# Kernel optimization log

Measured on AMD Instinct MI355X. Metric: run time of the kernel, lower is better.

Reference implementation:

```python
import jax, jax.numpy as jnp
import numpy as np

N = 50000      # nodes per graph batch (per siamese side)
E = 500000     # edges per side
F_IN = 128     # input_channels
H = 128        # hidden_channels
OUT = 2        # output_channels
G = 512        # number of graphs in the batch


def setup_inputs() -> dict:
    key = jax.random.key(0)
    ks = jax.random.split(key, 16)

    def lin_w(k, fan_in, shape):
        lim = 1.0 / np.sqrt(fan_in)
        return jax.random.uniform(k, shape, jnp.float32, -lim, lim)

    return {
        "x1": jax.random.normal(ks[0], (N, F_IN), jnp.float32),
        "x2": jax.random.normal(ks[1], (N, F_IN), jnp.float32),
        "edge_index1": jax.random.randint(ks[2], (2, E), 0, N, jnp.int32),
        "edge_index2": jax.random.randint(ks[3], (2, E), 0, N, jnp.int32),
        "batch1": jnp.sort(jax.random.randint(ks[4], (N,), 0, G, jnp.int32)),
        "batch2": jnp.sort(jax.random.randint(ks[5], (N,), 0, G, jnp.int32)),
        "W1": lin_w(ks[6], F_IN, (F_IN, H)), "b1": jnp.zeros((H,), jnp.float32),
        "W2": lin_w(ks[7], H, (H, H)),       "b2": jnp.zeros((H,), jnp.float32),
        "W3": lin_w(ks[8], H, (H, H)),       "b3": jnp.zeros((H,), jnp.float32),
        "Wc1": lin_w(ks[9], 2 * H, (2 * H, 4 * H)), "bc1": jnp.zeros((4 * H,), jnp.float32),
        "Wc2": lin_w(ks[10], 4 * H, (4 * H, 2 * H)), "bc2": jnp.zeros((2 * H,), jnp.float32),
        "Wc3": lin_w(ks[11], 2 * H, (2 * H, OUT)),   "bc3": jnp.zeros((OUT,), jnp.float32),
        "num_graphs": G,
    }


def _gcn_layer(x, W, b, src, dst, dinv):
    # PyG GCNConv: linear transform, then deg^{-1/2} A_hat deg^{-1/2} aggregation + bias
    h = x @ W
    msg = h[src] * (dinv[src] * dinv[dst])[:, None]   # [E+N, H]
    return jax.ops.segment_sum(msg, dst, num_segments=x.shape[0]) + b


def _forward_once(x, edge_index, batch, W1, b1, W2, b2, W3, b3, num_graphs):
    n = x.shape[0]
    loop = jnp.arange(n, dtype=edge_index.dtype)
    src = jnp.concatenate([edge_index[0], loop])      # add self-loops
    dst = jnp.concatenate([edge_index[1], loop])
    deg = jax.ops.segment_sum(jnp.ones_like(dst, dtype=x.dtype), dst, num_segments=n)
    dinv = jax.lax.rsqrt(deg)                          # deg >= 1 due to self-loops
    h = jax.nn.relu(_gcn_layer(x, W1, b1, src, dst, dinv))
    h = jax.nn.relu(_gcn_layer(h, W2, b2, src, dst, dinv))
    h = _gcn_layer(h, W3, b3, src, dst, dinv)
    # global_mean_pool over batch indices
    s = jax.ops.segment_sum(h, batch, num_segments=num_graphs)
    cnt = jax.ops.segment_sum(jnp.ones((n,), x.dtype), batch, num_segments=num_graphs)
    return s / jnp.maximum(cnt, 1.0)[:, None]


def reference(x1, x2, edge_index1, edge_index2, batch1, batch2,
              W1, b1, W2, b2, W3, b3, Wc1, bc1, Wc2, bc2, Wc3, bc3, num_graphs):
    g1 = _forward_once(x1, edge_index1, batch1, W1, b1, W2, b2, W3, b3, num_graphs)
    g2 = _forward_once(x2, edge_index2, batch2, W1, b1, W2, b2, W3, b3, num_graphs)
    z = jnp.concatenate([g1, g2], axis=1)             # [G, 2H]
    z = jax.nn.relu(z @ Wc1 + bc1)
    z = jax.nn.relu(z @ Wc2 + bc2)
    # dropout p=0.5 is identity at eval time
    return z @ Wc3 + bc3                               # [G, OUT]
```

## Files before the change

### kernel.cpp

```cpp
#include <hip/hip_runtime.h>
#include <math.h>

#define N_NODES 50000
#define E_EDGES 500000
#define HDIM    128
#define OUTC    2
#define NGRAPH  512

typedef _Float16 f16x8 __attribute__((ext_vector_type(8)));
typedef float    f32x4 __attribute__((ext_vector_type(4)));

__global__ void k_prep(const float* __restrict__ W1, const float* __restrict__ W2,
                       _Float16* __restrict__ w1hi, _Float16* __restrict__ w1lo,
                       _Float16* __restrict__ w2hi, _Float16* __restrict__ w2lo) {
    int i = blockIdx.x * blockDim.x + threadIdx.x;
    int stride = gridDim.x * blockDim.x;
    for (int j = i; j < 128 * 128; j += stride) {
        int n = j >> 7, k = j & 127;
        float v = W1[k * 128 + n];
        _Float16 h = (_Float16)v;
        w1hi[j] = h; w1lo[j] = (_Float16)(v - (float)h);
        v = W2[k * 128 + n];
        h = (_Float16)v;
        w2hi[j] = h; w2lo[j] = (_Float16)(v - (float)h);
    }
}

__global__ void k_hist(const int* __restrict__ d0, const int* __restrict__ d1,
                       int ecnt, int off1, int* __restrict__ cnt) {
    int i = blockIdx.x * blockDim.x + threadIdx.x;
    int stride = gridDim.x * blockDim.x;
    for (; i < ecnt; i += stride) {
        int d = (i < E_EDGES) ? d0[i] : d1[i - E_EDGES] + off1;
        atomicAdd(&cnt[d], 1);
    }
}

__global__ void k_scan_a(const int* __restrict__ cnt, int* __restrict__ excl,
                         int* __restrict__ blksum, float* __restrict__ dinv,
                         const int* __restrict__ bt0, const int* __restrict__ bt1,
                         int goff0, int nn, int nside, float* __restrict__ cnt_g) {
    __shared__ int s[512];
    int t = threadIdx.x;
    int i = blockIdx.x * 512 + t;
    int v = 0;
    if (i < nn) {
        v = cnt[i];
        dinv[i] = 1.0f / sqrtf((float)(v + 1));
        int g = (i < nside) ? bt0[i] + goff0 : bt1[i - nside] + NGRAPH;
        atomicAdd(&cnt_g[g], 1.0f);
    }
    s[t] = v; __syncthreads();
    for (int off = 1; off < 512; off <<= 1) {
        int add = (t >= off) ? s[t - off] : 0;
        __syncthreads();
        s[t] += add;
        __syncthreads();
    }
    if (i < nn) excl[i] = s[t] - v;
    if (t == 511) blksum[blockIdx.x] = s[511];
}

__global__ void k_scan_b(int* __restrict__ blksum, int nb) {
    __shared__ int s[512];
    int t = threadIdx.x;
    int v = (t < nb) ? blksum[t] : 0;
    s[t] = v; __syncthreads();
    for (int off = 1; off < 512; off <<= 1) {
        int add = (t >= off) ? s[t - off] : 0;
        __syncthreads();
        s[t] += add;
        __syncthreads();
    }
    if (t < nb) blksum[t] = s[t] - v;
}

__global__ void k_scan_c(int* __restrict__ excl, const int* __restrict__ blksum,
                         int* __restrict__ cursor, int nn, int tot) {
    int t = threadIdx.x;
    int i = blockIdx.x * 512 + t;
    if (i < nn) {
        int v = excl[i] + blksum[blockIdx.x];
        excl[i] = v;
        cursor[i] = v;
    }
    if (i == 0) excl[nn] = tot;
}

__global__ void k_fill(const int* __restrict__ s0, const int* __restrict__ s1,
                       const int* __restrict__ d0, const int* __restrict__ d1,
                       int ecnt, int off1, int goff0,
                       const int* __restrict__ bt0, const int* __restrict__ bt1,
                       int* __restrict__ cursor,
                       const float* __restrict__ dinv, int2* __restrict__ edges,
                       int* __restrict__ gdst) {
    int i = blockIdx.x * blockDim.x + threadIdx.x;
    int stride = gridDim.x * blockDim.x;
    for (; i < ecnt; i += stride) {
        int d, sg, g;
        if (i < E_EDGES) {
            int dl = d0[i];
            sg = s0[i]; d = dl; g = bt0[dl] + goff0;
        } else {
            int dl = d1[i - E_EDGES];
            sg = s1[i - E_EDGES] + off1; d = dl + off1; g = bt1[dl] + NGRAPH;
        }
        int p = atomicAdd(&cursor[d], 1);
        float w = dinv[sg] * dinv[d];
        edges[p] = make_int2(sg, __float_as_int(w));
        gdst[p] = g;
    }
}

__device__ inline void cvt8(const float4& p, const float4& q, f16x8& h, f16x8& l) {
    float v[8] = {p.x, p.y, p.z, p.w, q.x, q.y, q.z, q.w};
#pragma unroll
    for (int i = 0; i < 8; i++) {
        _Float16 hh = (_Float16)v[i];
        h[i] = hh;
        l[i] = (_Float16)(v[i] - (float)hh);
    }
}

template <int ASRC>
__global__ __launch_bounds__(256) void k_gemm_split(
        const float* __restrict__ A0f, const float* __restrict__ A1f, int nside,
        const _Float16* __restrict__ Ahi, const _Float16* __restrict__ Alo,
        const _Float16* __restrict__ Bhi, const _Float16* __restrict__ Blo,
        float* __restrict__ C, int M) {
    __shared__ _Float16 sA[2][128][40];
    __shared__ _Float16 sB[2][128][40];
    int tid = threadIdx.x;
    int wave = tid >> 6, lane = tid & 63;
    int wm = (wave >> 1) * 64;
    int wn = (wave & 1) * 64;
    int quad = lane >> 4, fm = lane & 15;
    int row0 = blockIdx.x * 128;

    int lr = tid >> 2;
    int lk = (tid & 3) * 8;

    f32x4 acc[4][4] = {};
    const float4 z4 = make_float4(0.f, 0.f, 0.f, 0.f);

    for (int kc = 0; kc < 128; kc += 32) {
        int r1 = row0 + lr, r2 = row0 + lr + 64;
        bool ok1 = r1 < M, ok2 = r2 < M;
        f16x8 ah1, al1, ah2, al2;
        if (ASRC == 1) {
            const float* p1 = (r1 < nside) ? A0f + (size_t)r1 * 128
                                           : A1f + (size_t)(r1 - nside) * 128;
            const float* p2 = (r2 < nside) ? A0f + (size_t)r2 * 128
                                           : A1f + (size_t)(r2 - nside) * 128;
            float4 a = ok1 ? *(const float4*)(p1 + kc + lk) : z4;
            float4 b = ok1 ? *(const float4*)(p1 + kc + lk + 4) : z4;
            float4 c = ok2 ? *(const float4*)(p2 + kc + lk) : z4;
            float4 d = ok2 ? *(const float4*)(p2 + kc + lk + 4) : z4;
            cvt8(a, b, ah1, al1);
            cvt8(c, d, ah2, al2);
        } else {
            const f16x8 zf = {};
            ah1 = ok1 ? *(const f16x8*)(Ahi + (size_t)r1 * 128 + kc + lk) : zf;
            al1 = ok1 ? *(const f16x8*)(Alo + (size_t)r1 * 128 + kc + lk) : zf;
            ah2 = ok2 ? *(const f16x8*)(Ahi + (size_t)r2 * 128 + kc + lk) : zf;
            al2 = ok2 ? *(const f16x8*)(Alo + (size_t)r2 * 128 + kc + lk) : zf;
        }
        f16x8 bh1 = *(const f16x8*)(Bhi + (size_t)lr * 128 + kc + lk);
        f16x8 bl1 = *(const f16x8*)(Blo + (size_t)lr * 128 + kc + lk);
        f16x8 bh2 = *(const f16x8*)(Bhi + (size_t)(lr + 64) * 128 + kc + lk);
        f16x8 bl2 = *(const f16x8*)(Blo + (size_t)(lr + 64) * 128 + kc + lk);
        __syncthreads();
        *(f16x8*)&sA[0][lr][lk]      = ah1;
        *(f16x8*)&sA[1][lr][lk]      = al1;
        *(f16x8*)&sA[0][lr + 64][lk] = ah2;
        *(f16x8*)&sA[1][lr + 64][lk] = al2;
        *(f16x8*)&sB[0][lr][lk]      = bh1;
        *(f16x8*)&sB[1][lr][lk]      = bl1;
        *(f16x8*)&sB[0][lr + 64][lk] = bh2;
        *(f16x8*)&sB[1][lr + 64][lk] = bl2;
        __syncthreads();

        f16x8 afh[4], afl[4], bfh[4], bfl[4];
#pragma unroll
        for (int mi = 0; mi < 4; mi++) {
            afh[mi] = *(const f16x8*)&sA[0][wm + mi * 16 + fm][quad * 8];
            afl[mi] = *(const f16x8*)&sA[1][wm + mi * 16 + fm][quad * 8];
        }
#pragma unroll
        for (int ni = 0; ni < 4; ni++) {
            bfh[ni] = *(const f16x8*)&sB[0][wn + ni * 16 + fm][quad * 8];
            bfl[ni] = *(const f16x8*)&sB[1][wn + ni * 16 + fm][quad * 8];
        }
#pragma unroll
        for (int mi = 0; mi < 4; mi++)
#pragma unroll
            for (int ni = 0; ni < 4; ni++) {
                acc[mi][ni] = __builtin_amdgcn_mfma_f32_16x16x32_f16(afh[mi], bfh[ni], acc[mi][ni], 0, 0, 0);
                acc[mi][ni] = __builtin_amdgcn_mfma_f32_16x16x32_f16(afh[mi], bfl[ni], acc[mi][ni], 0, 0, 0);
                acc[mi][ni] = __builtin_amdgcn_mfma_f32_16x16x32_f16(afl[mi], bfh[ni], acc[mi][ni], 0, 0, 0);
            }
    }

#pragma unroll
    for (int mi = 0; mi < 4; mi++)
#pragma unroll
        for (int reg = 0; reg < 4; reg++) {
            int r = row0 + wm + mi * 16 + quad * 4 + reg;
            if (r >= M) continue;
#pragma unroll
            for (int ni = 0; ni < 4; ni++)
                C[(size_t)r * 128 + wn + ni * 16 + fm] = acc[mi][ni][reg];
        }
}

__global__ __launch_bounds__(256) void k_gemm(
        const float* __restrict__ A, const float* __restrict__ B,
        const float* __restrict__ bias, float* __restrict__ C,
        int M, int Nn, int K, int ldc, int act) {
    __shared__ float As[16][64];
    __shared__ float Bs[16][68];
    int tid = threadIdx.x;
    int tx = tid & 15, ty = tid >> 4;
    int row0 = blockIdx.x * 64, col0 = blockIdx.y * 64;
    float acc[4][4] = {};
    int arow = tid >> 2;
    int acol = (tid & 3) * 4;
    int brow = tid >> 4;
    int bcol = (tid & 15) * 4;

    for (int k0 = 0; k0 < K; k0 += 16) {
        float4 av = make_float4(0.f, 0.f, 0.f, 0.f);
        int ar = row0 + arow;
        if (ar < M) av = *(const float4*)(A + (size_t)ar * K + k0 + acol);
        As[acol + 0][arow] = av.x;
        As[acol + 1][arow] = av.y;
        As[acol + 2][arow] = av.z;
        As[acol + 3][arow] = av.w;

        float4 bv = make_float4(0.f, 0.f, 0.f, 0.f);
        const float* Brow = B + (size_t)(k0 + brow) * Nn;
        int bc = col0 + bcol;
        if (bc + 3 < Nn) {
            bv = *(const float4*)(Brow + bc);
        } else {
            if (bc     < Nn) bv.x = Brow[bc];
            if (bc + 1 < Nn) bv.y = Brow[bc + 1];
            if (bc + 2 < Nn) bv.z = Brow[bc + 2];
        }
        Bs[brow][bcol + 0] = bv.x;
        Bs[brow][bcol + 1] = bv.y;
        Bs[brow][bcol + 2] = bv.z;
        Bs[brow][bcol + 3] = bv.w;
        __syncthreads();

#pragma unroll
        for (int k = 0; k < 16; k++) {
            float4 a = *(const float4*)&As[k][ty * 4];
            float4 b = *(const float4*)&Bs[k][tx * 4];
            acc[0][0] += a.x * b.x; acc[0][1] += a.x * b.y; acc[0][2] += a.x * b.z; acc[0][3] += a.x * b.w;
            acc[1][0] += a.y * b.x; acc[1][1] += a.y * b.y; acc[1][2] += a.y * b.z; acc[1][3] += a.y * b.w;
            acc[2][0] += a.z * b.x; acc[2][1] += a.z * b.y; acc[2][2] += a.z * b.z; acc[2][3] += a.z * b.w;
            acc[3][0] += a.w * b.x; acc[3][1] += a.w * b.y; acc[3][2] += a.w * b.z; acc[3][3] += a.w * b.w;
        }
        __syncthreads();
    }

#pragma unroll
    for (int i = 0; i < 4; i++) {
        int r = row0 + ty * 4 + i;
        if (r >= M) continue;
#pragma unroll
        for (int j = 0; j < 4; j++) {
            int c = col0 + tx * 4 + j;
            if (c >= Nn) continue;
            float v = acc[i][j];
            if (bias) v += bias[c];
            if (act) v = fmaxf(v, 0.0f);
            C[(size_t)r * ldc + c] = v;
        }
    }
}

__global__ __launch_bounds__(256) void k_gemm_pool(
        const float* __restrict__ pool, const float* __restrict__ cnt_g,
        const float* __restrict__ W, const float* __restrict__ bias,
        float* __restrict__ zcat) {
    __shared__ float As[16][64];
    __shared__ float Bs[16][68];
    int side = blockIdx.z;
    const float* A = pool + (size_t)side * NGRAPH * HDIM;
    const float* cg = cnt_g + side * NGRAPH;
    int tid = threadIdx.x;
    int tx = tid & 15, ty = tid >> 4;
    int row0 = blockIdx.x * 64, col0 = blockIdx.y * 64;
    float acc[4][4] = {};
    int arow = tid >> 2;
    int acol = (tid & 3) * 4;
    int brow = tid >> 4;
    int bcol = (tid & 15) * 4;

    for (int k0 = 0; k0 < 128; k0 += 16) {
        int ar = row0 + arow;
        float sc = 1.0f / fmaxf(cg[ar], 1.0f);
        float4 av = *(const float4*)(A + (size_t)ar * 128 + k0 + acol);
        As[acol + 0][arow] = av.x * sc;
        As[acol + 1][arow] = av.y * sc;
        As[acol + 2][arow] = av.z * sc;
        As[acol + 3][arow] = av.w * sc;

        float4 bv = *(const float4*)(W + (size_t)(k0 + brow) * 128 + col0 + bcol);
        Bs[brow][bcol + 0] = bv.x;
        Bs[brow][bcol + 1] = bv.y;
        Bs[brow][bcol + 2] = bv.z;
        Bs[brow][bcol + 3] = bv.w;
        __syncthreads();

#pragma unroll
        for (int k = 0; k < 16; k++) {
            float4 a = *(const float4*)&As[k][ty * 4];
            float4 b = *(const float4*)&Bs[k][tx * 4];
            acc[0][0] += a.x * b.x; acc[0][1] += a.x * b.y; acc[0][2] += a.x * b.z; acc[0][3] += a.x * b.w;
            acc[1][0] += a.y * b.x; acc[1][1] += a.y * b.y; acc[1][2] += a.y * b.z; acc[1][3] += a.y * b.w;
            acc[2][0] += a.z * b.x; acc[2][1] += a.z * b.y; acc[2][2] += a.z * b.z; acc[2][3] += a.z * b.w;
            acc[3][0] += a.w * b.x; acc[3][1] += a.w * b.y; acc[3][2] += a.w * b.z; acc[3][3] += a.w * b.w;
        }
        __syncthreads();
    }

#pragma unroll
    for (int i = 0; i < 4; i++) {
        int r = row0 + ty * 4 + i;
#pragma unroll
        for (int j = 0; j < 4; j++) {
            int c = col0 + tx * 4 + j;
            zcat[(size_t)r * 256 + side * 128 + c] = acc[i][j] + bias[c];
        }
    }
}

template <int PACK>
__global__ __launch_bounds__(256) void k_agg(
        const float* __restrict__ H, const float* __restrict__ dinv,
        const int* __restrict__ row_ptr, const int2* __restrict__ edges,
        const float* __restrict__ bias,
        _Float16* __restrict__ outHi, _Float16* __restrict__ outLo,
        float* __restrict__ outF, int nnodes) {
    int wave = threadIdx.x >> 6, lane = threadIdx.x & 63;
    int node = blockIdx.x * 4 + wave;
    if (node >= nnodes) return;

    float di = dinv[node];
    float2 hv = ((const float2*)(H + (size_t)node * HDIM))[lane];
    float wself = di * di;
    float ax = hv.x * wself;
    float ay = hv.y * wself;

    int rs = __builtin_amdgcn_readfirstlane(row_ptr[node]);
    int re = __builtin_amdgcn_readfirstlane(row_ptr[node + 1]);

    for (int base = rs; base < re; base += 8) {
        int nrem = re - base, m = nrem - 1;
        int i1 = 1 < nrem ? 1 : m;
        int i2 = 2 < nrem ? 2 : m;
        int i3 = 3 < nrem ? 3 : m;
        int i4 = 4 < nrem ? 4 : m;
        int i5 = 5 < nrem ? 5 : m;
        int i6 = 6 < nrem ? 6 : m;
        int i7 = 7 < nrem ? 7 : m;
        int2 E0 = edges[base];
        int2 E1 = edges[base + i1];
        int2 E2 = edges[base + i2];
        int2 E3 = edges[base + i3];
        int2 E4 = edges[base + i4];
        int2 E5 = edges[base + i5];
        int2 E6 = edges[base + i6];
        int2 E7 = edges[base + i7];
        float2 v0 = ((const float2*)(H + (size_t)E0.x * HDIM))[lane];
        float2 v1 = ((const float2*)(H + (size_t)E1.x * HDIM))[lane];
        float2 v2 = ((const float2*)(H + (size_t)E2.x * HDIM))[lane];
        float2 v3 = ((const float2*)(H + (size_t)E3.x * HDIM))[lane];
        float2 v4 = ((const float2*)(H + (size_t)E4.x * HDIM))[lane];
        float2 v5 = ((const float2*)(H + (size_t)E5.x * HDIM))[lane];
        float2 v6 = ((const float2*)(H + (size_t)E6.x * HDIM))[lane];
        float2 v7 = ((const float2*)(H + (size_t)E7.x * HDIM))[lane];
        float w0 = __int_as_float(E0.y);
        float w1 = 1 < nrem ? __int_as_float(E1.y) : 0.f;
        float w2 = 2 < nrem ? __int_as_float(E2.y) : 0.f;
        float w3 = 3 < nrem ? __int_as_float(E3.y) : 0.f;
        float w4 = 4 < nrem ? __int_as_float(E4.y) : 0.f;
        float w5 = 5 < nrem ? __int_as_float(E5.y) : 0.f;
        float w6 = 6 < nrem ? __int_as_float(E6.y) : 0.f;
        float w7 = 7 < nrem ? __int_as_float(E7.y) : 0.f;
        ax = fmaf(v0.x, w0, ax); ay = fmaf(v0.y, w0, ay);
        ax = fmaf(v1.x, w1, ax); ay = fmaf(v1.y, w1, ay);
        ax = fmaf(v2.x, w2, ax); ay = fmaf(v2.y, w2, ay);
        ax = fmaf(v3.x, w3, ax); ay = fmaf(v3.y, w3, ay);
        ax = fmaf(v4.x, w4, ax); ay = fmaf(v4.y, w4, ay);
        ax = fmaf(v5.x, w5, ax); ay = fmaf(v5.y, w5, ay);
        ax = fmaf(v6.x, w6, ax); ay = fmaf(v6.y, w6, ay);
        ax = fmaf(v7.x, w7, ax); ay = fmaf(v7.y, w7, ay);
    }

    float ox = fmaxf(ax + bias[lane * 2],     0.0f);
    float oy = fmaxf(ay + bias[lane * 2 + 1], 0.0f);
    if (PACK) {
        _Float16 hx = (_Float16)ox, hy = (_Float16)oy;
        _Float16 lx = (_Float16)(ox - (float)hx), ly = (_Float16)(oy - (float)hy);
        union { _Float16 h[2]; unsigned u; } ph, pl;
        ph.h[0] = hx; ph.h[1] = hy;
        pl.h[0] = lx; pl.h[1] = ly;
        ((unsigned*)(outHi + (size_t)node * HDIM))[lane] = ph.u;
        ((unsigned*)(outLo + (size_t)node * HDIM))[lane] = pl.u;
    } else {
        ((float2*)(outF + (size_t)node * HDIM))[lane] = make_float2(ox, oy);
    }
}

__global__ __launch_bounds__(256) void k_sweep3(
        const float* __restrict__ H, const int2* __restrict__ edges,
        const int* __restrict__ gdst, const float* __restrict__ dinv,
        const int* __restrict__ bt0, const int* __restrict__ bt1,
        int goff0, int nnodes, int nside, int nedges,
        float* __restrict__ pool) {
    int lane = threadIdx.x & 63;
    int wid = blockIdx.x * 4 + (threadIdx.x >> 6);
    int ewaves = (nedges + 63) >> 6;

    float ax = 0.f, ay = 0.f;

    if (wid < ewaves) {
        int e0 = wid << 6;
        int e1 = e0 + 64; if (e1 > nedges) e1 = nedges;
        int gcur = __builtin_amdgcn_readfirstlane(gdst[e0]);
        for (int base = e0; base < e1; base += 8) {
            int nrem = e1 - base, m = nrem - 1;
            int i1 = 1 < nrem ? 1 : m;
            int i2 = 2 < nrem ? 2 : m;
            int i3 = 3 < nrem ? 3 : m;
            int i4 = 4 < nrem ? 4 : m;
            int i5 = 5 < nrem ? 5 : m;
            int i6 = 6 < nrem ? 6 : m;
            int i7 = 7 < nrem ? 7 : m;
            int2 E0 = edges[base];
            int2 E1 = edges[base + i1];
            int2 E2 = edges[base + i2];
            int2 E3 = edges[base + i3];
            int2 E4 = edges[base + i4];
            int2 E5 = edges[base + i5];
            int2 E6 = edges[base + i6];
            int2 E7 = edges[base + i7];
            int g0 = __builtin_amdgcn_readfirstlane(gdst[base]);
            int g1 = __builtin_amdgcn_readfirstlane(gdst[base + i1]);
            int g2 = __builtin_amdgcn_readfirstlane(gdst[base + i2]);
            int g3 = __builtin_amdgcn_readfirstlane(gdst[base + i3]);
            int g4 = __builtin_amdgcn_readfirstlane(gdst[base + i4]);
            int g5 = __builtin_amdgcn_readfirstlane(gdst[base + i5]);
            int g6 = __builtin_amdgcn_readfirstlane(gdst[base + i6]);
            int g7 = __builtin_amdgcn_readfirstlane(gdst[base + i7]);
            float2 v0 = ((const float2*)(H + (size_t)E0.x * HDIM))[lane];
            float2 v1 = ((const float2*)(H + (size_t)E1.x * HDIM))[lane];
            float2 v2 = ((const float2*)(H + (size_t)E2.x * HDIM))[lane];
            float2 v3 = ((const float2*)(H + (size_t)E3.x * HDIM))[lane];
            float2 v4 = ((const float2*)(H + (size_t)E4.x * HDIM))[lane];
            float2 v5 = ((const float2*)(H + (size_t)E5.x * HDIM))[lane];
            float2 v6 = ((const float2*)(H + (size_t)E6.x * HDIM))[lane];
            float2 v7 = ((const float2*)(H + (size_t)E7.x * HDIM))[lane];
            float w0 = __int_as_float(E0.y);
            float w1 = 1 < nrem ? __int_as_float(E1.y) : 0.f;
            float w2 = 2 < nrem ? __int_as_float(E2.y) : 0.f;
            float w3 = 3 < nrem ? __int_as_float(E3.y) : 0.f;
            float w4 = 4 < nrem ? __int_as_float(E4.y) : 0.f;
            float w5 = 5 < nrem ? __int_as_float(E5.y) : 0.f;
            float w6 = 6 < nrem ? __int_as_float(E6.y) : 0.f;
            float w7 = 7 < nrem ? __int_as_float(E7.y) : 0.f;

            if ((g0 | g1 | g2 | g3 | g4 | g5 | g6 | g7) ==
                (g0 & g1 & g2 & g3 & g4 & g5 & g6 & g7) && g0 == gcur) {
                ax = fmaf(v0.x, w0, ax); ay = fmaf(v0.y, w0, ay);
                ax = fmaf(v1.x, w1, ax); ay = fmaf(v1.y, w1, ay);
                ax = fmaf(v2.x, w2, ax); ay = fmaf(v2.y, w2, ay);
                ax = fmaf(v3.x, w3, ax); ay = fmaf(v3.y, w3, ay);
                ax = fmaf(v4.x, w4, ax); ay = fmaf(v4.y, w4, ay);
                ax = fmaf(v5.x, w5, ax); ay = fmaf(v5.y, w5, ay);
                ax = fmaf(v6.x, w6, ax); ay = fmaf(v6.y, w6, ay);
                ax = fmaf(v7.x, w7, ax); ay = fmaf(v7.y, w7, ay);
            } else {
                int   gg[8] = {g0, g1, g2, g3, g4, g5, g6, g7};
                float wx[8] = {w0, w1, w2, w3, w4, w5, w6, w7};
                float2 vv[8] = {v0, v1, v2, v3, v4, v5, v6, v7};
#pragma unroll
                for (int j = 0; j < 8; j++) {
                    if (wx[j] != 0.f && gg[j] != gcur) {
                        float* p = pool + (size_t)gcur * HDIM + lane * 2;
                        atomicAdd(p, ax); atomicAdd(p + 1, ay);
                        ax = 0.f; ay = 0.f;
                        gcur = gg[j];
                    }
                    ax = fmaf(vv[j].x, wx[j], ax);
                    ay = fmaf(vv[j].y, wx[j], ay);
                }
            }
        }
        float* p = pool + (size_t)gcur * HDIM + lane * 2;
        atomicAdd(p, ax); atomicAdd(p + 1, ay);
    } else {
        int wid2 = wid - ewaves;
        int n0 = wid2 << 6;
        if (n0 >= nnodes) return;
        int n1 = n0 + 64; if (n1 > nnodes) n1 = nnodes;
        int gcur = (n0 < nside) ? bt0[n0] + goff0 : bt1[n0 - nside] + NGRAPH;
        gcur = __builtin_amdgcn_readfirstlane(gcur);
        for (int n = n0; n < n1; n++) {
            int g = (n < nside) ? bt0[n] + goff0 : bt1[n - nside] + NGRAPH;
            g = __builtin_amdgcn_readfirstlane(g);
            float dn = dinv[n];
            float w = dn * dn;
            float2 v = ((const float2*)(H + (size_t)n * HDIM))[lane];
            if (g != gcur) {
                float* p = pool + (size_t)gcur * HDIM + lane * 2;
                atomicAdd(p, ax); atomicAdd(p + 1, ay);
                ax = 0.f; ay = 0.f;
                gcur = g;
            }
            ax = fmaf(v.x, w, ax);
            ay = fmaf(v.y, w, ay);
        }
        float* p = pool + (size_t)gcur * HDIM + lane * 2;
        atomicAdd(p, ax); atomicAdd(p + 1, ay);
    }
}

extern "C" void kernel_launch(void* const* d_in, const int* in_sizes, int n_in,
                              void* d_out, int out_size, void* d_ws, size_t ws_size,
                              hipStream_t stream) {
    (void)in_sizes; (void)n_in; (void)out_size;

    const float* x[2]  = {(const float*)d_in[0], (const float*)d_in[1]};
    const int*   ei[2] = {(const int*)d_in[2], (const int*)d_in[3]};
    const int*   bt[2] = {(const int*)d_in[4], (const int*)d_in[5]};
    const float* W1  = (const float*)d_in[6];  const float* b1  = (const float*)d_in[7];
    const float* W2  = (const float*)d_in[8];  const float* b2  = (const float*)d_in[9];
    const float* W3  = (const float*)d_in[10]; const float* b3  = (const float*)d_in[11];
    const float* Wc1 = (const float*)d_in[12]; const float* bc1 = (const float*)d_in[13];
    const float* Wc2 = (const float*)d_in[14]; const float* bc2 = (const float*)d_in[15];
    const float* Wc3 = (const float*)d_in[16]; const float* bc3 = (const float*)d_in[17];
    float* out = (float*)d_out;

    const bool batched = ws_size >= 120ull * 1000 * 1000;
    const int NN = batched ? 2 * N_NODES : N_NODES;
    const int NE = batched ? 2 * E_EDGES : E_EDGES;

    char* ws = (char*)d_ws;
    size_t off = 0;
    auto carve = [&](size_t bytes) -> char* {
        char* p = ws + off;
        off += (bytes + 255) & ~(size_t)255;
        return p;
    };

    int*   edge_cnt = (int*)  carve((size_t)NN * 4);
    int*   cursor   = (int*)  carve((size_t)NN * 4);
    float* pool_s   = (float*)carve((size_t)2 * NGRAPH * HDIM * 4);
    float* cnt_g    = (float*)carve((size_t)2 * NGRAPH * 4);
    float* dinv     = (float*)carve((size_t)NN * 4);
    int*   row_ptr  = (int*)  carve((size_t)(NN + 1) * 4);
    int2*  edges    = (int2*) carve((size_t)NE * 8);
    int*   gdst     = (int*)  carve((size_t)NE * 4);
    int*   blksum   = (int*)  carve(1024 * 4);
    _Float16* wt    = (_Float16*)carve(4 * 128 * 128 * 2);
    _Float16* hS    = (_Float16*)carve((size_t)NN * HDIM * 4);
    float* hA       = (float*)carve((size_t)NN * HDIM * 4);
    float* zcat     = (float*)carve((size_t)NGRAPH * 2 * HDIM * 4);
    float* z1       = (float*)carve((size_t)NGRAPH * 4 * HDIM * 4);
    float* z2       = (float*)carve((size_t)NGRAPH * 2 * HDIM * 4);

    _Float16* w1hi = wt;
    _Float16* w1lo = wt + 128 * 128;
    _Float16* w2hi = wt + 2 * 128 * 128;
    _Float16* w2lo = wt + 3 * 128 * 128;
    _Float16* hShi = hS;
    _Float16* hSlo = hS + (size_t)NN * HDIM;
    float*    hSf  = (float*)hS;

    const int gblk = (NN + 127) / 128;
    const size_t poolz = (size_t)2 * NGRAPH * HDIM * 4 + (size_t)2 * NGRAPH * 4;

    hipMemsetAsync(pool_s, 0, poolz, stream);
    k_prep<<<64, 256, 0, stream>>>(W1, W2, w1hi, w1lo, w2hi, w2lo);

    if (batched) {
        const int nscan = (2 * N_NODES + 511) / 512;
        const int ablk  = (2 * N_NODES + 3) / 4;
        const int swaves = ((2 * E_EDGES + 63) >> 6) + ((2 * N_NODES + 63) >> 6);
        const int sblk = (swaves + 3) / 4;

        hipMemsetAsync(edge_cnt, 0, (size_t)NN * 4, stream);
        k_hist<<<1024, 256, 0, stream>>>(ei[0] + E_EDGES, ei[1] + E_EDGES,
                                         2 * E_EDGES, N_NODES, edge_cnt);
        k_scan_a<<<nscan, 512, 0, stream>>>(edge_cnt, row_ptr, blksum, dinv,
                                            bt[0], bt[1], 0, 2 * N_NODES, N_NODES, cnt_g);
        k_scan_b<<<1, 512, 0, stream>>>(blksum, nscan);
        k_scan_c<<<nscan, 512, 0, stream>>>(row_ptr, blksum, cursor, 2 * N_NODES, 2 * E_EDGES);
        k_fill<<<1024, 256, 0, stream>>>(ei[0], ei[1], ei[0] + E_EDGES, ei[1] + E_EDGES,
                                         2 * E_EDGES, N_NODES, 0, bt[0], bt[1],
                                         cursor, dinv, edges, gdst);

        k_gemm_split<1><<<gblk, 256, 0, stream>>>(x[0], x[1], N_NODES,
                                                  nullptr, nullptr, w1hi, w1lo, hA, 2 * N_NODES);
        k_agg<1><<<ablk, 256, 0, stream>>>(hA, dinv, row_ptr, edges, b1,
                                           hShi, hSlo, nullptr, 2 * N_NODES);
        k_gemm_split<0><<<gblk, 256, 0, stream>>>(nullptr, nullptr, 0,
                                                  hShi, hSlo, w2hi, w2lo, hA, 2 * N_NODES);
        k_agg<0><<<ablk, 256, 0, stream>>>(hA, dinv, row_ptr, edges, b2,
                                           nullptr, nullptr, hSf, 2 * N_NODES);
        k_sweep3<<<sblk, 256, 0, stream>>>(hSf, edges, gdst, dinv, bt[0], bt[1],
                                           0, 2 * N_NODES, N_NODES, 2 * E_EDGES, pool_s);
    } else {
        const int nscan = (N_NODES + 511) / 512;
        const int ablk  = (N_NODES + 3) / 4;
        const int swaves = ((E_EDGES + 63) >> 6) + ((N_NODES + 63) >> 6);
        const int sblk = (swaves + 3) / 4;

        for (int s = 0; s < 2; ++s) {
            const int* esrc = ei[s];
            const int* edst = ei[s] + E_EDGES;
            int goff = s * NGRAPH;

            hipMemsetAsync(edge_cnt, 0, (size_t)NN * 4, stream);
            k_hist<<<512, 256, 0, stream>>>(edst, edst, E_EDGES, 0, edge_cnt);
            k_scan_a<<<nscan, 512, 0, stream>>>(edge_cnt, row_ptr, blksum, dinv,
                                                bt[s], bt[s], goff, N_NODES, N_NODES, cnt_g);
            k_scan_b<<<1, 512, 0, stream>>>(blksum, nscan);
            k_scan_c<<<nscan, 512, 0, stream>>>(row_ptr, blksum, cursor, N_NODES, E_EDGES);
            k_fill<<<512, 256, 0, stream>>>(esrc, esrc, edst, edst, E_EDGES, 0, goff,
                                            bt[s], bt[s], cursor, dinv, edges, gdst);

            k_gemm_split<1><<<gblk, 256, 0, stream>>>(x[s], x[s], N_NODES,
                                                      nullptr, nullptr, w1hi, w1lo, hA, N_NODES);
            k_agg<1><<<ablk, 256, 0, stream>>>(hA, dinv, row_ptr, edges, b1,
                                               hShi, hSlo, nullptr, N_NODES);
            k_gemm_split<0><<<gblk, 256, 0, stream>>>(nullptr, nullptr, 0,
                                                      hShi, hSlo, w2hi, w2lo, hA, N_NODES);
            k_agg<0><<<ablk, 256, 0, stream>>>(hA, dinv, row_ptr, edges, b2,
                                               nullptr, nullptr, hSf, N_NODES);
            k_sweep3<<<sblk, 256, 0, stream>>>(hSf, edges, gdst, dinv, bt[s], bt[s],
                                               goff, N_NODES, N_NODES, E_EDGES, pool_s);
        }
    }

    k_gemm_pool<<<dim3(NGRAPH / 64, 2, 2), 256, 0, stream>>>(pool_s, cnt_g, W3, b3, zcat);

    k_gemm<<<dim3(NGRAPH / 64, (4 * HDIM) / 64), 256, 0, stream>>>(zcat, Wc1, bc1, z1, NGRAPH, 4 * HDIM, 2 * HDIM, 4 * HDIM, 1);
    k_gemm<<<dim3(NGRAPH / 64, (2 * HDIM) / 64), 256, 0, stream>>>(z1, Wc2, bc2, z2, NGRAPH, 2 * HDIM, 4 * HDIM, 2 * HDIM, 1);
    k_gemm<<<dim3(NGRAPH / 64, 1), 256, 0, stream>>>(z2, Wc3, bc3, out, NGRAPH, OUTC, 2 * HDIM, OUTC, 0);
}
```

Baseline: 678.3 us.

## Store GEMM outputs and layer-2 activations in fp16 to halve gather traffic

GEMM outputs (hA) and the layer-2 aggregate are now stored as fp16 instead of fp32, so the random neighbour gathers in k_agg and k_sweep3 read half as many bytes. The weight-split prep is folded into the histogram kernel, and the separate memsets are merged into one contiguous memset, which removes launches. k_sweep3 gains a fast path for 64-edge chunks whose first and last edge share a graph, and otherwise walks edges one at a time. Dropping to plain fp16 for these intermediates loses precision compared with the earlier hi/lo split scheme, so accuracy could suffer.

Result: faster. 589.2 us (-13.1%).

```diff
diff --git a/kernel.cpp b/kernel.cpp
--- a/kernel.cpp
+++ b/kernel.cpp
@@ -10,7 +10,19 @@
 typedef _Float16 f16x8 __attribute__((ext_vector_type(8)));
 typedef float    f32x4 __attribute__((ext_vector_type(4)));
 
-__global__ void k_prep(const float* __restrict__ W1, const float* __restrict__ W2,
+__device__ inline float2 unpack2(unsigned u) {
+    union { unsigned v; _Float16 h[2]; } c; c.v = u;
+    return make_float2((float)c.h[0], (float)c.h[1]);
+}
+__device__ inline unsigned pack2(float a, float b) {
+    union { _Float16 h[2]; unsigned u; } c;
+    c.h[0] = (_Float16)a; c.h[1] = (_Float16)b;
+    return c.u;
+}
+
+__global__ void k_hist(const int* __restrict__ d0, const int* __restrict__ d1,
+                       int ecnt, int off1, int* __restrict__ cnt,
+                       const float* __restrict__ W1, const float* __restrict__ W2,
                        _Float16* __restrict__ w1hi, _Float16* __restrict__ w1lo,
                        _Float16* __restrict__ w2hi, _Float16* __restrict__ w2lo) {
     int i = blockIdx.x * blockDim.x + threadIdx.x;
@@ -24,14 +36,8 @@
         h = (_Float16)v;
         w2hi[j] = h; w2lo[j] = (_Float16)(v - (float)h);
     }
-}
-
-__global__ void k_hist(const int* __restrict__ d0, const int* __restrict__ d1,
-                       int ecnt, int off1, int* __restrict__ cnt) {
-    int i = blockIdx.x * blockDim.x + threadIdx.x;
-    int stride = gridDim.x * blockDim.x;
-    for (; i < ecnt; i += stride) {
-        int d = (i < E_EDGES) ? d0[i] : d1[i - E_EDGES] + off1;
+    for (int j = i; j < ecnt; j += stride) {
+        int d = (j < E_EDGES) ? d0[j] : d1[j - E_EDGES] + off1;
         atomicAdd(&cnt[d], 1);
     }
 }
@@ -127,7 +133,7 @@
         const float* __restrict__ A0f, const float* __restrict__ A1f, int nside,
         const _Float16* __restrict__ Ahi, const _Float16* __restrict__ Alo,
         const _Float16* __restrict__ Bhi, const _Float16* __restrict__ Blo,
-        float* __restrict__ C, int M) {
+        _Float16* __restrict__ C, int M) {
     __shared__ _Float16 sA[2][128][40];
     __shared__ _Float16 sB[2][128][40];
     int tid = threadIdx.x;
@@ -209,7 +215,7 @@
             if (r >= M) continue;
 #pragma unroll
             for (int ni = 0; ni < 4; ni++)
-                C[(size_t)r * 128 + wn + ni * 16 + fm] = acc[mi][ni][reg];
+                C[(size_t)r * 128 + wn + ni * 16 + fm] = (_Float16)acc[mi][ni][reg];
         }
 }
 
@@ -340,17 +346,17 @@
 
 template <int PACK>
 __global__ __launch_bounds__(256) void k_agg(
-        const float* __restrict__ H, const float* __restrict__ dinv,
+        const _Float16* __restrict__ H, const float* __restrict__ dinv,
         const int* __restrict__ row_ptr, const int2* __restrict__ edges,
         const float* __restrict__ bias,
         _Float16* __restrict__ outHi, _Float16* __restrict__ outLo,
-        float* __restrict__ outF, int nnodes) {
+        int nnodes) {
     int wave = threadIdx.x >> 6, lane = threadIdx.x & 63;
     int node = blockIdx.x * 4 + wave;
     if (node >= nnodes) return;
 
     float di = dinv[node];
-    float2 hv = ((const float2*)(H + (size_t)node * HDIM))[lane];
+    float2 hv = unpack2(((const unsigned*)(H + (size_t)node * HDIM))[lane]);
     float wself = di * di;
     float ax = hv.x * wself;
     float ay = hv.y * wself;
@@ -375,14 +381,14 @@
         int2 E5 = edges[base + i5];
         int2 E6 = edges[base + i6];
         int2 E7 = edges[base + i7];
-        float2 v0 = ((const float2*)(H + (size_t)E0.x * HDIM))[lane];
-        float2 v1 = ((const float2*)(H + (size_t)E1.x * HDIM))[lane];
-        float2 v2 = ((const float2*)(H + (size_t)E2.x * HDIM))[lane];
-        float2 v3 = ((const float2*)(H + (size_t)E3.x * HDIM))[lane];
-        float2 v4 = ((const float2*)(H + (size_t)E4.x * HDIM))[lane];
-        float2 v5 = ((const float2*)(H + (size_t)E5.x * HDIM))[lane];
-        float2 v6 = ((const float2*)(H + (size_t)E6.x * HDIM))[lane];
-        float2 v7 = ((const float2*)(H + (size_t)E7.x * HDIM))[lane];
+        unsigned u0 = ((const unsigned*)(H + (size_t)E0.x * HDIM))[lane];
+        unsigned u1 = ((const unsigned*)(H + (size_t)E1.x * HDIM))[lane];
+        unsigned u2 = ((const unsigned*)(H + (size_t)E2.x * HDIM))[lane];
+        unsigned u3 = ((const unsigned*)(H + (size_t)E3.x * HDIM))[lane];
+        unsigned u4 = ((const unsigned*)(H + (size_t)E4.x * HDIM))[lane];
+        unsigned u5 = ((const unsigned*)(H + (size_t)E5.x * HDIM))[lane];
+        unsigned u6 = ((const unsigned*)(H + (size_t)E6.x * HDIM))[lane];
+        unsigned u7 = ((const unsigned*)(H + (size_t)E7.x * HDIM))[lane];
         float w0 = __int_as_float(E0.y);
         float w1 = 1 < nrem ? __int_as_float(E1.y) : 0.f;
         float w2 = 2 < nrem ? __int_as_float(E2.y) : 0.f;
@@ -391,6 +397,8 @@
         float w5 = 5 < nrem ? __int_as_float(E5.y) : 0.f;
         float w6 = 6 < nrem ? __int_as_float(E6.y) : 0.f;
         float w7 = 7 < nrem ? __int_as_float(E7.y) : 0.f;
+        float2 v0 = unpack2(u0), v1 = unpack2(u1), v2 = unpack2(u2), v3 = unpack2(u3);
+        float2 v4 = unpack2(u4), v5 = unpack2(u5), v6 = unpack2(u6), v7 = unpack2(u7);
         ax = fmaf(v0.x, w0, ax); ay = fmaf(v0.y, w0, ay);
         ax = fmaf(v1.x, w1, ax); ay = fmaf(v1.y, w1, ay);
         ax = fmaf(v2.x, w2, ax); ay = fmaf(v2.y, w2, ay);
@@ -412,12 +420,12 @@
         ((unsigned*)(outHi + (size_t)node * HDIM))[lane] = ph.u;
         ((unsigned*)(outLo + (size_t)node * HDIM))[lane] = pl.u;
     } else {
-        ((float2*)(outF + (size_t)node * HDIM))[lane] = make_float2(ox, oy);
+        ((unsigned*)(outHi + (size_t)node * HDIM))[lane] = pack2(ox, oy);
     }
 }
 
 __global__ __launch_bounds__(256) void k_sweep3(
-        const float* __restrict__ H, const int2* __restrict__ edges,
+        const _Float16* __restrict__ H, const int2* __restrict__ edges,
         const int* __restrict__ gdst, const float* __restrict__ dinv,
         const int* __restrict__ bt0, const int* __restrict__ bt1,
         int goff0, int nnodes, int nside, int nedges,
@@ -426,56 +434,49 @@
     int wid = blockIdx.x * 4 + (threadIdx.x >> 6);
     int ewaves = (nedges + 63) >> 6;
 
-    float ax = 0.f, ay = 0.f;
-
     if (wid < ewaves) {
         int e0 = wid << 6;
         int e1 = e0 + 64; if (e1 > nedges) e1 = nedges;
-        int gcur = __builtin_amdgcn_readfirstlane(gdst[e0]);
-        for (int base = e0; base < e1; base += 8) {
-            int nrem = e1 - base, m = nrem - 1;
-            int i1 = 1 < nrem ? 1 : m;
-            int i2 = 2 < nrem ? 2 : m;
-            int i3 = 3 < nrem ? 3 : m;
-            int i4 = 4 < nrem ? 4 : m;
-            int i5 = 5 < nrem ? 5 : m;
-            int i6 = 6 < nrem ? 6 : m;
-            int i7 = 7 < nrem ? 7 : m;
-            int2 E0 = edges[base];
-            int2 E1 = edges[base + i1];
-            int2 E2 = edges[base + i2];
-            int2 E3 = edges[base + i3];
-            int2 E4 = edges[base + i4];
-            int2 E5 = edges[base + i5];
-            int2 E6 = edges[base + i6];
-            int2 E7 = edges[base + i7];
-            int g0 = __builtin_amdgcn_readfirstlane(gdst[base]);
-            int g1 = __builtin_amdgcn_readfirstlane(gdst[base + i1]);
-            int g2 = __builtin_amdgcn_readfirstlane(gdst[base + i2]);
-            int g3 = __builtin_amdgcn_readfirstlane(gdst[base + i3]);
-            int g4 = __builtin_amdgcn_readfirstlane(gdst[base + i4]);
-            int g5 = __builtin_amdgcn_readfirstlane(gdst[base + i5]);
-            int g6 = __builtin_amdgcn_readfirstlane(gdst[base + i6]);
-            int g7 = __builtin_amdgcn_readfirstlane(gdst[base + i7]);
-            float2 v0 = ((const float2*)(H + (size_t)E0.x * HDIM))[lane];
-            float2 v1 = ((const float2*)(H + (size_t)E1.x * HDIM))[lane];
-            float2 v2 = ((const float2*)(H + (size_t)E2.x * HDIM))[lane];
-            float2 v3 = ((const float2*)(H + (size_t)E3.x * HDIM))[lane];
-            float2 v4 = ((const float2*)(H + (size_t)E4.x * HDIM))[lane];
-            float2 v5 = ((const float2*)(H + (size_t)E5.x * HDIM))[lane];
-            float2 v6 = ((const float2*)(H + (size_t)E6.x * HDIM))[lane];
-            float2 v7 = ((const float2*)(H + (size_t)E7.x * HDIM))[lane];
-            float w0 = __int_as_float(E0.y);
-            float w1 = 1 < nrem ? __int_as_float(E1.y) : 0.f;
-            float w2 = 2 < nrem ? __int_as_float(E2.y) : 0.f;
-            float w3 = 3 < nrem ? __int_as_float(E3.y) : 0.f;
-            float w4 = 4 < nrem ? __int_as_float(E4.y) : 0.f;
-            float w5 = 5 < nrem ? __int_as_float(E5.y) : 0.f;
-            float w6 = 6 < nrem ? __int_as_float(E6.y) : 0.f;
-            float w7 = 7 < nrem ? __int_as_float(E7.y) : 0.f;
-
-            if ((g0 | g1 | g2 | g3 | g4 | g5 | g6 | g7) ==
-                (g0 & g1 & g2 & g3 & g4 & g5 & g6 & g7) && g0 == gcur) {
+        int gfirst = __builtin_amdgcn_readfirstlane(gdst[e0]);
+        int glast  = __builtin_amdgcn_readfirstlane(gdst[e1 - 1]);
+        float ax = 0.f, ay = 0.f;
+
+        if (gfirst == glast) {
+            for (int base = e0; base < e1; base += 8) {
+                int nrem = e1 - base, m = nrem - 1;
+                int i1 = 1 < nrem ? 1 : m;
+                int i2 = 2 < nrem ? 2 : m;
+                int i3 = 3 < nrem ? 3 : m;
+                int i4 = 4 < nrem ? 4 : m;
+                int i5 = 5 < nrem ? 5 : m;
+                int i6 = 6 < nrem ? 6 : m;
+                int i7 = 7 < nrem ? 7 : m;
+                int2 E0 = edges[base];
+                int2 E1 = edges[base + i1];
+                int2 E2 = edges[base + i2];
+                int2 E3 = edges[base + i3];
+                int2 E4 = edges[base + i4];
+                int2 E5 = edges[base + i5];
+                int2 E6 = edges[base + i6];
+                int2 E7 = edges[base + i7];
+                unsigned u0 = ((const unsigned*)(H + (size_t)E0.x * HDIM))[lane];
+                unsigned u1 = ((const unsigned*)(H + (size_t)E1.x * HDIM))[lane];
+                unsigned u2 = ((const unsigned*)(H + (size_t)E2.x * HDIM))[lane];
+                unsigned u3 = ((const unsigned*)(H + (size_t)E3.x * HDIM))[lane];
+                unsigned u4 = ((const unsigned*)(H + (size_t)E4.x * HDIM))[lane];
+                unsigned u5 = ((const unsigned*)(H + (size_t)E5.x * HDIM))[lane];
+                unsigned u6 = ((const unsigned*)(H + (size_t)E6.x * HDIM))[lane];
+                unsigned u7 = ((const unsigned*)(H + (size_t)E7.x * HDIM))[lane];
+                float w0 = __int_as_float(E0.y);
+                float w1 = 1 < nrem ? __int_as_float(E1.y) : 0.f;
+                float w2 = 2 < nrem ? __int_as_float(E2.y) : 0.f;
+                float w3 = 3 < nrem ? __int_as_float(E3.y) : 0.f;
+                float w4 = 4 < nrem ? __int_as_float(E4.y) : 0.f;
+                float w5 = 5 < nrem ? __int_as_float(E5.y) : 0.f;
+                float w6 = 6 < nrem ? __int_as_float(E6.y) : 0.f;
+                float w7 = 7 < nrem ? __int_as_float(E7.y) : 0.f;
+                float2 v0 = unpack2(u0), v1 = unpack2(u1), v2 = unpack2(u2), v3 = unpack2(u3);
+                float2 v4 = unpack2(u4), v5 = unpack2(u5), v6 = unpack2(u6), v7 = unpack2(u7);
                 ax = fmaf(v0.x, w0, ax); ay = fmaf(v0.y, w0, ay);
                 ax = fmaf(v1.x, w1, ax); ay = fmaf(v1.y, w1, ay);
                 ax = fmaf(v2.x, w2, ax); ay = fmaf(v2.y, w2, ay);
@@ -484,30 +485,34 @@
                 ax = fmaf(v5.x, w5, ax); ay = fmaf(v5.y, w5, ay);
                 ax = fmaf(v6.x, w6, ax); ay = fmaf(v6.y, w6, ay);
                 ax = fmaf(v7.x, w7, ax); ay = fmaf(v7.y, w7, ay);
-            } else {
-                int   gg[8] = {g0, g1, g2, g3, g4, g5, g6, g7};
-                float wx[8] = {w0, w1, w2, w3, w4, w5, w6, w7};
-                float2 vv[8] = {v0, v1, v2, v3, v4, v5, v6, v7};
-#pragma unroll
-                for (int j = 0; j < 8; j++) {
-                    if (wx[j] != 0.f && gg[j] != gcur) {
-                        float* p = pool + (size_t)gcur * HDIM + lane * 2;
-                        atomicAdd(p, ax); atomicAdd(p + 1, ay);
-                        ax = 0.f; ay = 0.f;
-                        gcur = gg[j];
-                    }
-                    ax = fmaf(vv[j].x, wx[j], ax);
-                    ay = fmaf(vv[j].y, wx[j], ay);
+            }
+            float* p = pool + (size_t)gfirst * HDIM + lane * 2;
+            atomicAdd(p, ax); atomicAdd(p + 1, ay);
+        } else {
+            int gcur = gfirst;
+            for (int e = e0; e < e1; e++) {
+                int2 E = edges[e];
+                int g = __builtin_amdgcn_readfirstlane(gdst[e]);
+                if (g != gcur) {
+                    float* p = pool + (size_t)gcur * HDIM + lane * 2;
+                    atomicAdd(p, ax); atomicAdd(p + 1, ay);
+                    ax = 0.f; ay = 0.f;
+                    gcur = g;
                 }
+                float w = __int_as_float(E.y);
+                float2 v = unpack2(((const unsigned*)(H + (size_t)E.x * HDIM))[lane]);
+                ax = fmaf(v.x, w, ax);
+                ay = fmaf(v.y, w, ay);
             }
-        }
-        float* p = pool + (size_t)gcur * HDIM + lane * 2;
-        atomicAdd(p, ax); atomicAdd(p + 1, ay);
+            float* p = pool + (size_t)gcur * HDIM + lane * 2;
+            atomicAdd(p, ax); atomicAdd(p + 1, ay);
+        }
     } else {
         int wid2 = wid - ewaves;
         int n0 = wid2 << 6;
         if (n0 >= nnodes) return;
         int n1 = n0 + 64; if (n1 > nnodes) n1 = nnodes;
+        float ax = 0.f, ay = 0.f;
         int gcur = (n0 < nside) ? bt0[n0] + goff0 : bt1[n0 - nside] + NGRAPH;
         gcur = __builtin_amdgcn_readfirstlane(gcur);
         for (int n = n0; n < n1; n++) {
@@ -515,7 +520,7 @@
             g = __builtin_amdgcn_readfirstlane(g);
             float dn = dinv[n];
             float w = dn * dn;
-            float2 v = ((const float2*)(H + (size_t)n * HDIM))[lane];
+            float2 v = unpack2(((const unsigned*)(H + (size_t)n * HDIM))[lane]);
             if (g != gcur) {
                 float* p = pool + (size_t)gcur * HDIM + lane * 2;
                 atomicAdd(p, ax); atomicAdd(p + 1, ay);
@@ -569,7 +574,7 @@
     int*   blksum   = (int*)  carve(1024 * 4);
     _Float16* wt    = (_Float16*)carve(4 * 128 * 128 * 2);
     _Float16* hS    = (_Float16*)carve((size_t)NN * HDIM * 4);
-    float* hA       = (float*)carve((size_t)NN * HDIM * 4);
+    _Float16* hA    = (_Float16*)carve((size_t)NN * HDIM * 2);
     float* zcat     = (float*)carve((size_t)NGRAPH * 2 * HDIM * 4);
     float* z1       = (float*)carve((size_t)NGRAPH * 4 * HDIM * 4);
     float* z2       = (float*)carve((size_t)NGRAPH * 2 * HDIM * 4);
@@ -580,13 +585,10 @@
     _Float16* w2lo = wt + 3 * 128 * 128;
     _Float16* hShi = hS;
     _Float16* hSlo = hS + (size_t)NN * HDIM;
-    float*    hSf  = (float*)hS;
 
     const int gblk = (NN + 127) / 128;
-    const size_t poolz = (size_t)2 * NGRAPH * HDIM * 4 + (size_t)2 * NGRAPH * 4;
-
-    hipMemsetAsync(pool_s, 0, poolz, stream);
-    k_prep<<<64, 256, 0, stream>>>(W1, W2, w1hi, w1lo, w2hi, w2lo);
+    size_t zero_all = (size_t)((char*)cnt_g + 2 * NGRAPH * 4 - (char*)edge_cnt);
+    size_t zero_cnt = (size_t)((char*)pool_s - (char*)edge_cnt);
 
     if (batched) {
         const int nscan = (2 * N_NODES + 511) / 512;
@@ -594,9 +596,10 @@
         const int swaves = ((2 * E_EDGES + 63) >> 6) + ((2 * N_NODES + 63) >> 6);
         const int sblk = (swaves + 3) / 4;
 
-        hipMemsetAsync(edge_cnt, 0, (size_t)NN * 4, stream);
+        hipMemsetAsync(edge_cnt, 0, zero_all, stream);
         k_hist<<<1024, 256, 0, stream>>>(ei[0] + E_EDGES, ei[1] + E_EDGES,
-                                         2 * E_EDGES, N_NODES, edge_cnt);
+                                         2 * E_EDGES, N_NODES, edge_cnt,
+                                         W1, W2, w1hi, w1lo, w2hi, w2lo);
         k_scan_a<<<nscan, 512, 0, stream>>>(edge_cnt, row_ptr, blksum, dinv,
                                             bt[0], bt[1], 0, 2 * N_NODES, N_NODES, cnt_g);
         k_scan_b<<<1, 512, 0, stream>>>(blksum, nscan);
@@ -608,12 +611,12 @@
         k_gemm_split<1><<<gblk, 256, 0, stream>>>(x[0], x[1], N_NODES,
                                                   nullptr, nullptr, w1hi, w1lo, hA, 2 * N_NODES);
         k_agg<1><<<ablk, 256, 0, stream>>>(hA, dinv, row_ptr, edges, b1,
-                                           hShi, hSlo, nullptr, 2 * N_NODES);
+                                           hShi, hSlo, 2 * N_NODES);
         k_gemm_split<0><<<gblk, 256, 0, stream>>>(nullptr, nullptr, 0,
                                                   hShi, hSlo, w2hi, w2lo, hA, 2 * N_NODES);
         k_agg<0><<<ablk, 256, 0, stream>>>(hA, dinv, row_ptr, edges, b2,
-                                           nullptr, nullptr, hSf, 2 * N_NODES);
-        k_sweep3<<<sblk, 256, 0, stream>>>(hSf, edges, gdst, dinv, bt[0], bt[1],
+                                           hShi, nullptr, 2 * N_NODES);
+        k_sweep3<<<sblk, 256, 0, stream>>>(hShi, edges, gdst, dinv, bt[0], bt[1],
                                            0, 2 * N_NODES, N_NODES, 2 * E_EDGES, pool_s);
     } else {
         const int nscan = (N_NODES + 511) / 512;
@@ -626,8 +629,9 @@
             const int* edst = ei[s] + E_EDGES;
             int goff = s * NGRAPH;
 
-            hipMemsetAsync(edge_cnt, 0, (size_t)NN * 4, stream);
-            k_hist<<<512, 256, 0, stream>>>(edst, edst, E_EDGES, 0, edge_cnt);
+            hipMemsetAsync(edge_cnt, 0, s == 0 ? zero_all : zero_cnt, stream);
+            k_hist<<<512, 256, 0, stream>>>(edst, edst, E_EDGES, 0, edge_cnt,
+                                            W1, W2, w1hi, w1lo, w2hi, w2lo);
             k_scan_a<<<nscan, 512, 0, stream>>>(edge_cnt, row_ptr, blksum, dinv,
                                                 bt[s], bt[s], goff, N_NODES, N_NODES, cnt_g);
             k_scan_b<<<1, 512, 0, stream>>>(blksum, nscan);
@@ -638,12 +642,12 @@
             k_gemm_split<1><<<gblk, 256, 0, stream>>>(x[s], x[s], N_NODES,
                                                       nullptr, nullptr, w1hi, w1lo, hA, N_NODES);
             k_agg<1><<<ablk, 256, 0, stream>>>(hA, dinv, row_ptr, edges, b1,
-                                               hShi, hSlo, nullptr, N_NODES);
+                                               hShi, hSlo, N_NODES);
             k_gemm_split<0><<<gblk, 256, 0, stream>>>(nullptr, nullptr, 0,
                                                       hShi, hSlo, w2hi, w2lo, hA, N_NODES);
             k_agg<0><<<ablk, 256, 0, stream>>>(hA, dinv, row_ptr, edges, b2,
-                                               nullptr, nullptr, hSf, N_NODES);
-            k_sweep3<<<sblk, 256, 0, stream>>>(hSf, edges, gdst, dinv, bt[s], bt[s],
+                                               hShi, nullptr, N_NODES);
+            k_sweep3<<<sblk, 256, 0, stream>>>(hShi, edges, gdst, dinv, bt[s], bt[s],
                                                goff, N_NODES, N_NODES, E_EDGES, pool_s);
         }
     }
```
